# Optimization experiments

Hardware: AMD Instinct MI355X
Metric: run time of the kernel (lower is better)

Reference implementation:

```python
import jax, jax.numpy as jnp
import numpy as np

N = 262144   # nodes
E = 4194304  # edges (avg degree 16)
G = 1024     # graphs in batch
F_IN, F_GCN, F_DENSE = 3, 16, 16
NEG_SLOPE = 0.01  # nn.LeakyReLU default


def _leaky(x):
    return jax.nn.leaky_relu(x, NEG_SLOPE)


def _gcn_conv(x, W, b, src, dst, ew):
    """PyG GCNConv: h = x @ W; symmetric deg-norm with self-loops (weight 1);
    out[i] = sum_{(j->i)} norm_e * h[j] + (1/deg_i) * h[i] + b."""
    h = x @ W                                   # [N, out]
    deg = jax.ops.segment_sum(ew, dst, num_segments=N) + 1.0  # +1 from self-loop
    dinv = jnp.where(deg > 0, jax.lax.rsqrt(deg), 0.0)        # deg^{-1/2}
    norm = dinv[src] * ew * dinv[dst]           # [E]
    agg = jax.ops.segment_sum(h[src] * norm[:, None], dst, num_segments=N)
    agg = agg + h * (dinv * dinv)[:, None]      # self-loop message, norm = 1/deg
    return agg + b


def setup_inputs() -> dict:
    key = jax.random.key(0)
    ks = jax.random.split(key, 24)
    inp = {
        "X": jax.random.normal(ks[0], (N, F_IN), dtype=jnp.float32),
        "Edge_index": jax.random.randint(ks[1], (2, E), 0, N, dtype=jnp.int64) if jax.config.jax_enable_x64 else jax.random.randint(ks[1], (2, E), 0, N, dtype=jnp.int32),
        "Edge_weight": jax.random.uniform(ks[2], (E,), dtype=jnp.float32),
        "Batching": jnp.sort(jax.random.randint(ks[3], (N,), 0, G, dtype=jnp.int32)),
        "num_graphs": G,
    }
    def lin(k, fi, fo):
        kw, kb = jax.random.split(k)
        s = 1.0 / np.sqrt(fi)
        return (jax.random.uniform(kw, (fi, fo), minval=-s, maxval=s, dtype=jnp.float32),
                jax.random.uniform(kb, (fo,), minval=-s, maxval=s, dtype=jnp.float32))
    inp["W1"], inp["b1"] = lin(ks[4], F_IN, F_GCN)
    inp["W2"], inp["b2"] = lin(ks[5], F_GCN, F_GCN)
    inp["Wp1"], inp["bp1"] = lin(ks[6], F_GCN, F_DENSE)
    inp["Wp2"], inp["bp2"] = lin(ks[7], F_DENSE, F_DENSE)
    inp["Wp3"], inp["bp3"] = lin(ks[8], F_DENSE, 2)
    inp["Wt1"], inp["bt1"] = lin(ks[9], F_GCN, F_DENSE)
    inp["Wt2"], inp["bt2"] = lin(ks[10], F_DENSE, F_DENSE)
    inp["Wt3"], inp["bt3"] = lin(ks[11], F_DENSE, 2)
    return inp


def reference(X, Edge_index, Edge_weight, Batching, num_graphs,
              W1, b1, W2, b2,
              Wp1, bp1, Wp2, bp2, Wp3, bp3,
              Wt1, bt1, Wt2, bt2, Wt3, bt3):
    src, dst = Edge_index[0], Edge_index[1]
    out = _leaky(_gcn_conv(X, W1, b1, src, dst, Edge_weight))
    out = _leaky(_gcn_conv(out, W2, b2, src, dst, Edge_weight))
    # global mean pool over graphs
    sums = jax.ops.segment_sum(out, Batching, num_segments=num_graphs)
    cnt = jax.ops.segment_sum(jnp.ones((out.shape[0],), out.dtype), Batching,
                              num_segments=num_graphs)
    pooled = sums / jnp.maximum(cnt, 1.0)[:, None]   # [G, 16]
    Phi = _leaky(pooled @ Wp1 + bp1)
    Phi = _leaky(Phi @ Wp2 + bp2)
    Phi = Phi @ Wp3 + bp3
    Theta = _leaky(pooled @ Wt1 + bt1)
    Theta = _leaky(Theta @ Wt2 + bt2)
    Theta = Theta @ Wt3 + bt3
    return jnp.concatenate((Phi, Theta), axis=1)   # [G, 4]
```

## Files before the change

kernel.cpp:

```cpp
#include <hip/hip_runtime.h>


#define NBUCK 512
#define BCAP  10240
#define CHUNK 4096
#define NTILE 8
#define TSH   15
#define RCAP  20

__device__ __forceinline__ float leaky(float x) { return x > 0.f ? x : 0.01f * x; }

__global__ __launch_bounds__(256) void
binA_kernel(const int* __restrict__ src, const int* __restrict__ dst,
            const float* __restrict__ ew, int* __restrict__ bucketCursor,
            int2* __restrict__ coarse, int E) {
    __shared__ int lhist[NBUCK], lbase[NBUCK], lcur[NBUCK], gbase[NBUCK];
    __shared__ int tmp[256];
    __shared__ int2 stag[CHUNK];
    __shared__ unsigned short sbuck[CHUNK];
    int t = threadIdx.x;
    int base = blockIdx.x * CHUNK;
    for (int b = t; b < NBUCK; b += 256) { lhist[b] = 0; lcur[b] = 0; }
    __syncthreads();
    int n = min(CHUNK, E - base);
    int myDst[16], mySrc[16]; float myEw[16];
#pragma unroll
    for (int k = 0; k < 16; ++k) {
        int j = t + k * 256;
        if (j < n) {
            int d = dst[base + j];
            myDst[k] = d; mySrc[k] = src[base + j]; myEw[k] = ew[base + j];
            atomicAdd(&lhist[d >> 9], 1);
        } else myDst[k] = -1;
    }
    __syncthreads();
    tmp[t] = lhist[2 * t] + lhist[2 * t + 1];
    __syncthreads();
    for (int off = 1; off < 256; off <<= 1) {
        int v = (t >= off) ? tmp[t - off] : 0;
        __syncthreads();
        tmp[t] += v;
        __syncthreads();
    }
    int pb = (t == 0) ? 0 : tmp[t - 1];
    lbase[2 * t] = pb;
    lbase[2 * t + 1] = pb + lhist[2 * t];
    __syncthreads();
    for (int b = t; b < NBUCK; b += 256) {
        int c = lhist[b];
        gbase[b] = c ? atomicAdd(&bucketCursor[b], c) : 0;
    }
    for (int k = 0; k < 16; ++k) {
        int d = myDst[k];
        if (d >= 0) {
            int b = d >> 9;
            int p = lbase[b] + atomicAdd(&lcur[b], 1);
            stag[p] = make_int2(mySrc[k] | ((d & 511) << 18), __float_as_int(myEw[k]));
            sbuck[p] = (unsigned short)b;
        }
    }
    __syncthreads();
    for (int j = t; j < n; j += 256) {
        int b = sbuck[j];
        coarse[(size_t)b * BCAP + gbase[b] + (j - lbase[b])] = stag[j];
    }
}

__global__ void bscan_kernel(const int* __restrict__ bucketCursor,
                             int* __restrict__ bucketBase, int* __restrict__ row,
                             int N, int E) {
    __shared__ int s[NBUCK];
    int t = threadIdx.x;
    int v = bucketCursor[t];
    s[t] = v;
    __syncthreads();
    for (int off = 1; off < NBUCK; off <<= 1) {
        int x = (t >= off) ? s[t - off] : 0;
        __syncthreads();
        s[t] += x;
        __syncthreads();
    }
    bucketBase[t] = s[t] - v;
    if (t == 0) row[N] = E;
}

__global__ __launch_bounds__(512, 2) void
binB_kernel(const int* __restrict__ bucketCursor, const int* __restrict__ bucketBase,
            const int2* __restrict__ coarse, int2* __restrict__ edata,
            int* __restrict__ row, float* __restrict__ dinv,
            uint4* __restrict__ tcnt) {
    __shared__ int2 sedata[BCAP];
    __shared__ int loff[NBUCK * NTILE];
    __shared__ int tmp[512];
    int b = blockIdx.x, t = threadIdx.x;
    for (int i = t; i < NBUCK * NTILE; i += 512) loff[i] = 0;
    __syncthreads();
    int cnt = bucketCursor[b];
    int gb  = bucketBase[b];
    const int2* cb = coarse + (size_t)b * BCAP;
    int2 myE[RCAP]; int myKey[RCAP];
#pragma unroll
    for (int k = 0; k < RCAP; ++k) {
        int j = t + k * 512;
        if (j < cnt) {
            int2 e = cb[j];
            myE[k] = e;
            myKey[k] = (((e.x >> 18) & 511) << 3) | ((e.x & 0x3FFFF) >> TSH);
            atomicAdd(&loff[myKey[k]], 1);
        } else myKey[k] = -1;
    }
    __syncthreads();
    int base8 = t * 8, s = 0;
#pragma unroll
    for (int k = 0; k < 8; ++k) s += loff[base8 + k];
    tmp[t] = s;
    __syncthreads();
    for (int off = 1; off < 512; off <<= 1) {
        int v = (t >= off) ? tmp[t - off] : 0;
        __syncthreads();
        tmp[t] += v;
        __syncthreads();
    }
    int run = tmp[t] - s;
    int o[9];
#pragma unroll
    for (int k = 0; k < 8; ++k) { int v = loff[base8 + k]; o[k] = run; loff[base8 + k] = run; run += v; }
    o[8] = run;
    __syncthreads();
    int node = b * 512 + t;
    row[node] = gb + o[0];
    uint4 p;
    p.x = (unsigned)(o[1] - o[0]) | ((unsigned)(o[2] - o[1]) << 16);
    p.y = (unsigned)(o[3] - o[2]) | ((unsigned)(o[4] - o[3]) << 16);
    p.z = (unsigned)(o[5] - o[4]) | ((unsigned)(o[6] - o[5]) << 16);
    p.w = (unsigned)(o[7] - o[6]) | ((unsigned)(o[8] - o[7]) << 16);
    tcnt[node] = p;
#pragma unroll
    for (int k = 0; k < RCAP; ++k) {
        if (myKey[k] >= 0) {
            int pos = atomicAdd(&loff[myKey[k]], 1);
            sedata[pos] = make_int2(myE[k].x & 0x3FFFF, myE[k].y);
        }
    }
    __syncthreads();
    for (int j = t; j < cnt; j += 512) edata[gb + j] = sedata[j];
    float dsum = 0.f;
    for (int j = o[0]; j < o[8]; ++j) dsum += __int_as_float(sedata[j].y);
    dinv[node] = rsqrtf(1.0f + dsum);
}

__global__ void pack_kernel(const float* __restrict__ X, const float* __restrict__ dinv,
                            float4* __restrict__ Xp, int N) {
    int i = blockIdx.x * blockDim.x + threadIdx.x;
    if (i >= N) return;
    Xp[i] = make_float4(X[3 * i], X[3 * i + 1], X[3 * i + 2], dinv[i]);
}

__global__ __launch_bounds__(512) void
aggA_kernel(const int* __restrict__ row, const int2* __restrict__ edata,
            const float4* __restrict__ Xp, const float* __restrict__ W1,
            const float* __restrict__ b1, const float* __restrict__ W2,
            float* __restrict__ h2) {
    __shared__ float w1s[48];
    __shared__ float w[256];
    __shared__ float bb[16];
    __shared__ float sx[128][17];
    int t = threadIdx.x;
    if (t < 256) w[t] = W2[t];
    else if (t < 272) bb[t - 256] = b1[t - 256];
    else if (t >= 288 && t < 336) w1s[t - 288] = W1[t - 288];
    __syncthreads();
    int ln = t >> 2, l = t & 3;
    float w1r0[4], w1r1[4], w1r2[4];
#pragma unroll
    for (int c = 0; c < 4; ++c) {
        w1r0[c] = w1s[0 * 16 + 4 * l + c];
        w1r1[c] = w1s[1 * 16 + 4 * l + c];
        w1r2[c] = w1s[2 * 16 + 4 * l + c];
    }
    int iA = blockIdx.x * 256 + ln, iB = iA + 128;
    int eA = row[iA], eAend = row[iA + 1];
    int eB = row[iB], eBend = row[iB + 1];
    float4 xpA = Xp[iA], xpB = Xp[iB];
    float diA = xpA.w, diB = xpB.w;
    float accA[4], accB[4];
#pragma unroll
    for (int c = 0; c < 4; ++c) {
        accA[c] = (xpA.x * w1r0[c] + xpA.y * w1r1[c] + xpA.z * w1r2[c]) * diA;
        accB[c] = (xpB.x * w1r0[c] + xpB.y * w1r1[c] + xpB.z * w1r2[c]) * diB;
    }
    while (eA < eAend || eB < eBend) {
        if (eA < eAend) {
            int2 ed = edata[eA++];
            float4 xs = Xp[ed.x];
            float f = __int_as_float(ed.y) * xs.w;
            float f0 = xs.x * f, f1 = xs.y * f, f2 = xs.z * f;
#pragma unroll
            for (int c = 0; c < 4; ++c)
                accA[c] += f0 * w1r0[c] + f1 * w1r1[c] + f2 * w1r2[c];
        }
        if (eB < eBend) {
            int2 ed = edata[eB++];
            float4 xs = Xp[ed.x];
            float f = __int_as_float(ed.y) * xs.w;
            float f0 = xs.x * f, f1 = xs.y * f, f2 = xs.z * f;
#pragma unroll
            for (int c = 0; c < 4; ++c)
                accB[c] += f0 * w1r0[c] + f1 * w1r1[c] + f2 * w1r2[c];
        }
    }
    sx[ln][4 * l + 0] = leaky(diA * accA[0] + bb[4 * l + 0]);
    sx[ln][4 * l + 1] = leaky(diA * accA[1] + bb[4 * l + 1]);
    sx[ln][4 * l + 2] = leaky(diA * accA[2] + bb[4 * l + 2]);
    sx[ln][4 * l + 3] = leaky(diA * accA[3] + bb[4 * l + 3]);
    __syncthreads();
    {
        float a0 = 0.f, a1 = 0.f, a2 = 0.f, a3 = 0.f;
#pragma unroll
        for (int q = 0; q < 16; ++q) {
            float xv = sx[ln][q];
            a0 += xv * w[q * 16 + 4 * l + 0];
            a1 += xv * w[q * 16 + 4 * l + 1];
            a2 += xv * w[q * 16 + 4 * l + 2];
            a3 += xv * w[q * 16 + 4 * l + 3];
        }
        ((float4*)h2)[(size_t)iA * 4 + l] = make_float4(a0 * diA, a1 * diA, a2 * diA, a3 * diA);
    }
    __syncthreads();
    sx[ln][4 * l + 0] = leaky(diB * accB[0] + bb[4 * l + 0]);
    sx[ln][4 * l + 1] = leaky(diB * accB[1] + bb[4 * l + 1]);
    sx[ln][4 * l + 2] = leaky(diB * accB[2] + bb[4 * l + 2]);
    sx[ln][4 * l + 3] = leaky(diB * accB[3] + bb[4 * l + 3]);
    __syncthreads();
    {
        float a0 = 0.f, a1 = 0.f, a2 = 0.f, a3 = 0.f;
#pragma unroll
        for (int q = 0; q < 16; ++q) {
            float xv = sx[ln][q];
            a0 += xv * w[q * 16 + 4 * l + 0];
            a1 += xv * w[q * 16 + 4 * l + 1];
            a2 += xv * w[q * 16 + 4 * l + 2];
            a3 += xv * w[q * 16 + 4 * l + 3];
        }
        ((float4*)h2)[(size_t)iB * 4 + l] = make_float4(a0 * diB, a1 * diB, a2 * diB, a3 * diB);
    }
}

__global__ __launch_bounds__(512) void
aggB_kernel(const int* __restrict__ row, const uint4* __restrict__ tcnt,
            const int2* __restrict__ edata, const float* __restrict__ dinv,
            const float* __restrict__ h2prime, float* __restrict__ agg2) {
    int t = threadIdx.x;
    int ln = t >> 2, l = t & 3;
    int iA = blockIdx.x * 256 + ln, iB = iA + 128;
    const float4* hp = (const float4*)h2prime;
    int eA = row[iA], eB = row[iB];
    uint4 cAv = tcnt[iA], cBv = tcnt[iB];
    unsigned ca[4] = {cAv.x, cAv.y, cAv.z, cAv.w};
    unsigned cb[4] = {cBv.x, cBv.y, cBv.z, cBv.w};
    float diA = dinv[iA], diB = dinv[iB];
    float4 accA = hp[(size_t)iA * 4 + l];
    float4 accB = hp[(size_t)iB * 4 + l];
#pragma unroll
    for (int tt = 0; tt < NTILE; ++tt) {
        int nA = (ca[tt >> 1] >> ((tt & 1) * 16)) & 0xFFFF;
        int nB = (cb[tt >> 1] >> ((tt & 1) * 16)) & 0xFFFF;
        for (int e = eA + nA; eA < e; ++eA) {
            int2 ed = edata[eA];
            float ewv = __int_as_float(ed.y);
            float4 v = hp[(size_t)ed.x * 4 + l];
            accA.x += v.x * ewv; accA.y += v.y * ewv;
            accA.z += v.z * ewv; accA.w += v.w * ewv;
        }
        for (int e = eB + nB; eB < e; ++eB) {
            int2 ed = edata[eB];
            float ewv = __int_as_float(ed.y);
            float4 v = hp[(size_t)ed.x * 4 + l];
            accB.x += v.x * ewv; accB.y += v.y * ewv;
            accB.z += v.z * ewv; accB.w += v.w * ewv;
        }
        __syncthreads();
    }
    ((float4*)agg2)[(size_t)iA * 4 + l] =
        make_float4(accA.x * diA, accA.y * diA, accA.z * diA, accA.w * diA);
    ((float4*)agg2)[(size_t)iB * 4 + l] =
        make_float4(accB.x * diB, accB.y * diB, accB.z * diB, accB.w * diB);
}

__device__ void head_mlp(const float* pooled,
                         const float* __restrict__ Wa, const float* __restrict__ ba,
                         const float* __restrict__ Wb, const float* __restrict__ bb,
                         const float* __restrict__ Wc, const float* __restrict__ bc,
                         float* o) {
    float t[16], u[16];
#pragma unroll
    for (int f = 0; f < 16; ++f) {
        float a = ba[f];
        for (int k = 0; k < 16; ++k) a += pooled[k] * Wa[k * 16 + f];
        t[f] = leaky(a);
    }
#pragma unroll
    for (int f = 0; f < 16; ++f) {
        float a = bb[f];
        for (int k = 0; k < 16; ++k) a += t[k] * Wb[k * 16 + f];
        u[f] = leaky(a);
    }
    float o0 = bc[0], o1 = bc[1];
    for (int k = 0; k < 16; ++k) { o0 += u[k] * Wc[2 * k]; o1 += u[k] * Wc[2 * k + 1]; }
    o[0] = o0; o[1] = o1;
}

__global__ void pool_head_kernel(const float* __restrict__ agg2, const float* __restrict__ b2,
                                 const int* __restrict__ batching, int N,
                                 const float* __restrict__ Wp1, const float* __restrict__ bp1,
                                 const float* __restrict__ Wp2, const float* __restrict__ bp2,
                                 const float* __restrict__ Wp3, const float* __restrict__ bp3,
                                 const float* __restrict__ Wt1, const float* __restrict__ bt1,
                                 const float* __restrict__ Wt2, const float* __restrict__ bt2,
                                 const float* __restrict__ Wt3, const float* __restrict__ bt3,
                                 float* __restrict__ out) {
    int g = blockIdx.x;
    __shared__ int bounds[2];
    if (threadIdx.x < 2) {
        int v = g + (int)threadIdx.x;
        int lo = 0, hi = N;
        while (lo < hi) { int m = (lo + hi) >> 1; if (batching[m] < v) lo = m + 1; else hi = m; }
        bounds[threadIdx.x] = lo;
    }
    __syncthreads();
    int lo = bounds[0], hi = bounds[1];
    int f = threadIdx.x & 15, r = threadIdx.x >> 4;
    float bf = b2[f];
    float acc = 0.f;
    for (int i = lo + r; i < hi; i += 16) acc += leaky(agg2[(size_t)i * 16 + f] + bf);
    __shared__ float red[16][17];
    red[r][f] = acc;
    __syncthreads();
    __shared__ float pooled[16];
    if (r == 0) {
        float s = 0.f;
#pragma unroll
        for (int k = 0; k < 16; ++k) s += red[k][f];
        pooled[f] = s / fmaxf((float)(hi - lo), 1.0f);
    }
    __syncthreads();
    if (threadIdx.x == 0) {
        float o[2];
        head_mlp(pooled, Wp1, bp1, Wp2, bp2, Wp3, bp3, o);
        out[4 * g + 0] = o[0]; out[4 * g + 1] = o[1];
    } else if (threadIdx.x == 1) {
        float o[2];
        head_mlp(pooled, Wt1, bt1, Wt2, bt2, Wt3, bt3, o);
        out[4 * g + 2] = o[0]; out[4 * g + 3] = o[1];
    }
}

extern "C" void kernel_launch(void* const* d_in, const int* in_sizes, int n_in,
                              void* d_out, int out_size, void* d_ws, size_t ws_size,
                              hipStream_t stream) {
    const float* X        = (const float*)d_in[0];
    const int*   ei       = (const int*)d_in[1];
    const float* ew       = (const float*)d_in[2];
    const int*   batching = (const int*)d_in[3];
    const float* W1  = (const float*)d_in[5];  const float* b1  = (const float*)d_in[6];
    const float* W2  = (const float*)d_in[7];  const float* b2  = (const float*)d_in[8];
    const float* Wp1 = (const float*)d_in[9];  const float* bp1 = (const float*)d_in[10];
    const float* Wp2 = (const float*)d_in[11]; const float* bp2 = (const float*)d_in[12];
    const float* Wp3 = (const float*)d_in[13]; const float* bp3 = (const float*)d_in[14];
    const float* Wt1 = (const float*)d_in[15]; const float* bt1 = (const float*)d_in[16];
    const float* Wt2 = (const float*)d_in[17]; const float* bt2 = (const float*)d_in[18];
    const float* Wt3 = (const float*)d_in[19]; const float* bt3 = (const float*)d_in[20];

    const int N = in_sizes[3];
    const int E = in_sizes[2];
    const int G = out_size / 4;
    const int* src = ei;
    const int* dst = ei + E;

    char* ws = (char*)d_ws;
    size_t off = 0;
    int2*  edata = (int2*)(ws + off);  off += (size_t)E * 8;
    char*  regionA = ws + off;         off += (size_t)N * 64 * 3;
    int2*  coarse = (int2*)regionA;
    float* h2     = (float*)regionA;
    float* agg2   = (float*)(regionA + (size_t)N * 64);
    float4* Xp    = (float4*)(regionA + (size_t)N * 128);
    int*   bucketCursor = (int*)(ws + off); off += NBUCK * 4;
    int*   bucketBase   = (int*)(ws + off); off += NBUCK * 4;
    int*   row   = (int*)(ws + off);   off += (size_t)(N + 4) * 4;
    float* dinv  = (float*)(ws + off); off += (size_t)N * 4;
    uint4* tcnt  = (uint4*)(ws + off); off += (size_t)N * 16;
    float* out   = (float*)d_out;

    hipMemsetAsync(bucketCursor, 0, NBUCK * 4, stream);

    const int tb = 256;
    binA_kernel<<<(E + CHUNK - 1) / CHUNK, tb, 0, stream>>>(src, dst, ew, bucketCursor, coarse, E);
    bscan_kernel<<<1, NBUCK, 0, stream>>>(bucketCursor, bucketBase, row, N, E);
    binB_kernel<<<NBUCK, 512, 0, stream>>>(bucketCursor, bucketBase, coarse, edata, row, dinv, tcnt);
    pack_kernel<<<(N + tb - 1) / tb, tb, 0, stream>>>(X, dinv, Xp, N);
    aggA_kernel<<<N / 256, 512, 0, stream>>>(row, edata, Xp, W1, b1, W2, h2);
    aggB_kernel<<<N / 256, 512, 0, stream>>>(row, tcnt, edata, dinv, h2, agg2);
    pool_head_kernel<<<G, tb, 0, stream>>>(agg2, b2, batching, N,
                                           Wp1, bp1, Wp2, bp2, Wp3, bp3,
                                           Wt1, bt1, Wt2, bt2, Wt3, bt3, out);
}
```

Baseline: 382.4 us.

## Tile-synchronize first-layer gather and use nontemporal edge loads and output stores

The first GCN aggregation kernel now walks each node's edges in per-source-tile segments taken from the tcnt counts, with a block barrier after each tile. This mirrors the second aggregation kernel and keeps the block's gathers of Xp confined to one source range at a time, so they stay cache-resident. Both aggregation kernels also read edge records with nontemporal loads and write h2 and agg2 with nontemporal stores, to keep the streamed data from evicting the gathered feature rows. The extra barriers can stall warps whose nodes have uneven per-tile degrees.

```diff
diff --git a/kernel.cpp b/kernel.cpp
--- a/kernel.cpp
+++ b/kernel.cpp
@@ -9,6 +9,18 @@
 #define RCAP  20
 
 __device__ __forceinline__ float leaky(float x) { return x > 0.f ? x : 0.01f * x; }
+
+typedef float __attribute__((ext_vector_type(4))) f32x4;
+
+__device__ __forceinline__ void nt_store4(float a, float b, float c, float d, float* dst) {
+    f32x4 v = {a, b, c, d};
+    __builtin_nontemporal_store(v, (f32x4*)dst);
+}
+__device__ __forceinline__ void nt_edge(const int2* p, int& s, float& w) {
+    long long raw = __builtin_nontemporal_load((const long long*)p);
+    s = (int)(unsigned)(raw & 0xFFFFFFFFll);
+    w = __int_as_float((int)(raw >> 32));
+}
 
 __global__ __launch_bounds__(256) void
 binA_kernel(const int* __restrict__ src, const int* __restrict__ dst,
@@ -157,10 +169,10 @@
 }
 
 __global__ __launch_bounds__(512) void
-aggA_kernel(const int* __restrict__ row, const int2* __restrict__ edata,
-            const float4* __restrict__ Xp, const float* __restrict__ W1,
-            const float* __restrict__ b1, const float* __restrict__ W2,
-            float* __restrict__ h2) {
+aggA_kernel(const int* __restrict__ row, const uint4* __restrict__ tcnt,
+            const int2* __restrict__ edata, const float4* __restrict__ Xp,
+            const float* __restrict__ W1, const float* __restrict__ b1,
+            const float* __restrict__ W2, float* __restrict__ h2) {
     __shared__ float w1s[48];
     __shared__ float w[256];
     __shared__ float bb[16];
@@ -179,8 +191,10 @@
         w1r2[c] = w1s[2 * 16 + 4 * l + c];
     }
     int iA = blockIdx.x * 256 + ln, iB = iA + 128;
-    int eA = row[iA], eAend = row[iA + 1];
-    int eB = row[iB], eBend = row[iB + 1];
+    int eA = row[iA], eB = row[iB];
+    uint4 cAv = tcnt[iA], cBv = tcnt[iB];
+    unsigned ca[4] = {cAv.x, cAv.y, cAv.z, cAv.w};
+    unsigned cb[4] = {cBv.x, cBv.y, cBv.z, cBv.w};
     float4 xpA = Xp[iA], xpB = Xp[iB];
     float diA = xpA.w, diB = xpB.w;
     float accA[4], accB[4];
@@ -189,25 +203,29 @@
         accA[c] = (xpA.x * w1r0[c] + xpA.y * w1r1[c] + xpA.z * w1r2[c]) * diA;
         accB[c] = (xpB.x * w1r0[c] + xpB.y * w1r1[c] + xpB.z * w1r2[c]) * diB;
     }
-    while (eA < eAend || eB < eBend) {
-        if (eA < eAend) {
-            int2 ed = edata[eA++];
-            float4 xs = Xp[ed.x];
-            float f = __int_as_float(ed.y) * xs.w;
+#pragma unroll
+    for (int tt = 0; tt < NTILE; ++tt) {
+        int nA = (ca[tt >> 1] >> ((tt & 1) * 16)) & 0xFFFF;
+        int nB = (cb[tt >> 1] >> ((tt & 1) * 16)) & 0xFFFF;
+        for (int e = eA + nA; eA < e; ++eA) {
+            int s; float ewv; nt_edge(edata + eA, s, ewv);
+            float4 xs = Xp[s];
+            float f = ewv * xs.w;
             float f0 = xs.x * f, f1 = xs.y * f, f2 = xs.z * f;
 #pragma unroll
             for (int c = 0; c < 4; ++c)
                 accA[c] += f0 * w1r0[c] + f1 * w1r1[c] + f2 * w1r2[c];
         }
-        if (eB < eBend) {
-            int2 ed = edata[eB++];
-            float4 xs = Xp[ed.x];
-            float f = __int_as_float(ed.y) * xs.w;
+        for (int e = eB + nB; eB < e; ++eB) {
+            int s; float ewv; nt_edge(edata + eB, s, ewv);
+            float4 xs = Xp[s];
+            float f = ewv * xs.w;
             float f0 = xs.x * f, f1 = xs.y * f, f2 = xs.z * f;
 #pragma unroll
             for (int c = 0; c < 4; ++c)
                 accB[c] += f0 * w1r0[c] + f1 * w1r1[c] + f2 * w1r2[c];
         }
+        __syncthreads();
     }
     sx[ln][4 * l + 0] = leaky(diA * accA[0] + bb[4 * l + 0]);
     sx[ln][4 * l + 1] = leaky(diA * accA[1] + bb[4 * l + 1]);
@@ -224,7 +242,7 @@
             a2 += xv * w[q * 16 + 4 * l + 2];
             a3 += xv * w[q * 16 + 4 * l + 3];
         }
-        ((float4*)h2)[(size_t)iA * 4 + l] = make_float4(a0 * diA, a1 * diA, a2 * diA, a3 * diA);
+        nt_store4(a0 * diA, a1 * diA, a2 * diA, a3 * diA, h2 + (size_t)iA * 16 + l * 4);
     }
     __syncthreads();
     sx[ln][4 * l + 0] = leaky(diB * accB[0] + bb[4 * l + 0]);
@@ -242,7 +260,7 @@
             a2 += xv * w[q * 16 + 4 * l + 2];
             a3 += xv * w[q * 16 + 4 * l + 3];
         }
-        ((float4*)h2)[(size_t)iB * 4 + l] = make_float4(a0 * diB, a1 * diB, a2 * diB, a3 * diB);
+        nt_store4(a0 * diB, a1 * diB, a2 * diB, a3 * diB, h2 + (size_t)iB * 16 + l * 4);
     }
 }
 
@@ -266,25 +284,23 @@
         int nA = (ca[tt >> 1] >> ((tt & 1) * 16)) & 0xFFFF;
         int nB = (cb[tt >> 1] >> ((tt & 1) * 16)) & 0xFFFF;
         for (int e = eA + nA; eA < e; ++eA) {
-            int2 ed = edata[eA];
-            float ewv = __int_as_float(ed.y);
-            float4 v = hp[(size_t)ed.x * 4 + l];
+            int s; float ewv; nt_edge(edata + eA, s, ewv);
+            float4 v = hp[(size_t)s * 4 + l];
             accA.x += v.x * ewv; accA.y += v.y * ewv;
             accA.z += v.z * ewv; accA.w += v.w * ewv;
         }
         for (int e = eB + nB; eB < e; ++eB) {
-            int2 ed = edata[eB];
-            float ewv = __int_as_float(ed.y);
-            float4 v = hp[(size_t)ed.x * 4 + l];
+            int s; float ewv; nt_edge(edata + eB, s, ewv);
+            float4 v = hp[(size_t)s * 4 + l];
             accB.x += v.x * ewv; accB.y += v.y * ewv;
             accB.z += v.z * ewv; accB.w += v.w * ewv;
         }
         __syncthreads();
     }
-    ((float4*)agg2)[(size_t)iA * 4 + l] =
-        make_float4(accA.x * diA, accA.y * diA, accA.z * diA, accA.w * diA);
-    ((float4*)agg2)[(size_t)iB * 4 + l] =
-        make_float4(accB.x * diB, accB.y * diB, accB.z * diB, accB.w * diB);
+    nt_store4(accA.x * diA, accA.y * diA, accA.z * diA, accA.w * diA,
+              agg2 + (size_t)iA * 16 + l * 4);
+    nt_store4(accB.x * diB, accB.y * diB, accB.z * diB, accB.w * diB,
+              agg2 + (size_t)iB * 16 + l * 4);
 }
 
 __device__ void head_mlp(const float* pooled,
@@ -399,7 +415,7 @@
     bscan_kernel<<<1, NBUCK, 0, stream>>>(bucketCursor, bucketBase, row, N, E);
     binB_kernel<<<NBUCK, 512, 0, stream>>>(bucketCursor, bucketBase, coarse, edata, row, dinv, tcnt);
     pack_kernel<<<(N + tb - 1) / tb, tb, 0, stream>>>(X, dinv, Xp, N);
-    aggA_kernel<<<N / 256, 512, 0, stream>>>(row, edata, Xp, W1, b1, W2, h2);
+    aggA_kernel<<<N / 256, 512, 0, stream>>>(row, tcnt, edata, Xp, W1, b1, W2, h2);
     aggB_kernel<<<N / 256, 512, 0, stream>>>(row, tcnt, edata, dinv, h2, agg2);
     pool_head_kernel<<<G, tb, 0, stream>>>(agg2, b2, batching, N,
                                            Wp1, bp1, Wp2, bp2, Wp3, bp3,
```

Result: slower. 429.5 us (+12.3%).

## Enlarge binning blocks and tile aggA edge loop by source range with block sync

Applied to the files above, without the earlier changes.

The edge-binning kernel now runs 512 threads over 8192-edge chunks, so each bucket maps to one thread and the two-per-thread scan is dropped. The first aggregation kernel now walks each node's edges in eight source-range tiles, using per-tile counts already computed for aggB, with a block barrier after each tile. The barrier keeps the block's gathers of Xp within a narrow source window for better cache locality. In exchange it adds synchronization, and load imbalance inside a tile now stalls the whole block.

```diff
diff --git a/kernel.cpp b/kernel.cpp
--- a/kernel.cpp
+++ b/kernel.cpp
@@ -3,30 +3,31 @@
 
 #define NBUCK 512
 #define BCAP  10240
-#define CHUNK 4096
+#define CHUNK 8192
+#define APT   16
 #define NTILE 8
 #define TSH   15
 #define RCAP  20
 
 __device__ __forceinline__ float leaky(float x) { return x > 0.f ? x : 0.01f * x; }
 
-__global__ __launch_bounds__(256) void
+__global__ __launch_bounds__(512) void
 binA_kernel(const int* __restrict__ src, const int* __restrict__ dst,
             const float* __restrict__ ew, int* __restrict__ bucketCursor,
             int2* __restrict__ coarse, int E) {
     __shared__ int lhist[NBUCK], lbase[NBUCK], lcur[NBUCK], gbase[NBUCK];
-    __shared__ int tmp[256];
+    __shared__ int tmp[NBUCK];
     __shared__ int2 stag[CHUNK];
     __shared__ unsigned short sbuck[CHUNK];
     int t = threadIdx.x;
     int base = blockIdx.x * CHUNK;
-    for (int b = t; b < NBUCK; b += 256) { lhist[b] = 0; lcur[b] = 0; }
+    lhist[t] = 0; lcur[t] = 0;
     __syncthreads();
     int n = min(CHUNK, E - base);
-    int myDst[16], mySrc[16]; float myEw[16];
-#pragma unroll
-    for (int k = 0; k < 16; ++k) {
-        int j = t + k * 256;
+    int myDst[APT], mySrc[APT]; float myEw[APT];
+#pragma unroll
+    for (int k = 0; k < APT; ++k) {
+        int j = t + k * 512;
         if (j < n) {
             int d = dst[base + j];
             myDst[k] = d; mySrc[k] = src[base + j]; myEw[k] = ew[base + j];
@@ -34,23 +35,20 @@
         } else myDst[k] = -1;
     }
     __syncthreads();
-    tmp[t] = lhist[2 * t] + lhist[2 * t + 1];
-    __syncthreads();
-    for (int off = 1; off < 256; off <<= 1) {
+    int hv = lhist[t];
+    tmp[t] = hv;
+    __syncthreads();
+    for (int off = 1; off < NBUCK; off <<= 1) {
         int v = (t >= off) ? tmp[t - off] : 0;
         __syncthreads();
         tmp[t] += v;
         __syncthreads();
     }
-    int pb = (t == 0) ? 0 : tmp[t - 1];
-    lbase[2 * t] = pb;
-    lbase[2 * t + 1] = pb + lhist[2 * t];
-    __syncthreads();
-    for (int b = t; b < NBUCK; b += 256) {
-        int c = lhist[b];
-        gbase[b] = c ? atomicAdd(&bucketCursor[b], c) : 0;
-    }
-    for (int k = 0; k < 16; ++k) {
+    lbase[t] = tmp[t] - hv;
+    gbase[t] = hv ? atomicAdd(&bucketCursor[t], hv) : 0;
+    __syncthreads();
+#pragma unroll
+    for (int k = 0; k < APT; ++k) {
         int d = myDst[k];
         if (d >= 0) {
             int b = d >> 9;
@@ -60,7 +58,7 @@
         }
     }
     __syncthreads();
-    for (int j = t; j < n; j += 256) {
+    for (int j = t; j < n; j += 512) {
         int b = sbuck[j];
         coarse[(size_t)b * BCAP + gbase[b] + (j - lbase[b])] = stag[j];
     }
@@ -157,10 +155,10 @@
 }
 
 __global__ __launch_bounds__(512) void
-aggA_kernel(const int* __restrict__ row, const int2* __restrict__ edata,
-            const float4* __restrict__ Xp, const float* __restrict__ W1,
-            const float* __restrict__ b1, const float* __restrict__ W2,
-            float* __restrict__ h2) {
+aggA_kernel(const int* __restrict__ row, const uint4* __restrict__ tcnt,
+            const int2* __restrict__ edata, const float4* __restrict__ Xp,
+            const float* __restrict__ W1, const float* __restrict__ b1,
+            const float* __restrict__ W2, float* __restrict__ h2) {
     __shared__ float w1s[48];
     __shared__ float w[256];
     __shared__ float bb[16];
@@ -179,8 +177,10 @@
         w1r2[c] = w1s[2 * 16 + 4 * l + c];
     }
     int iA = blockIdx.x * 256 + ln, iB = iA + 128;
-    int eA = row[iA], eAend = row[iA + 1];
-    int eB = row[iB], eBend = row[iB + 1];
+    int eA = row[iA], eB = row[iB];
+    uint4 cAv = tcnt[iA], cBv = tcnt[iB];
+    unsigned ca[4] = {cAv.x, cAv.y, cAv.z, cAv.w};
+    unsigned cb[4] = {cBv.x, cBv.y, cBv.z, cBv.w};
     float4 xpA = Xp[iA], xpB = Xp[iB];
     float diA = xpA.w, diB = xpB.w;
     float accA[4], accB[4];
@@ -189,9 +189,12 @@
         accA[c] = (xpA.x * w1r0[c] + xpA.y * w1r1[c] + xpA.z * w1r2[c]) * diA;
         accB[c] = (xpB.x * w1r0[c] + xpB.y * w1r1[c] + xpB.z * w1r2[c]) * diB;
     }
-    while (eA < eAend || eB < eBend) {
-        if (eA < eAend) {
-            int2 ed = edata[eA++];
+#pragma unroll
+    for (int tt = 0; tt < NTILE; ++tt) {
+        int nA = (ca[tt >> 1] >> ((tt & 1) * 16)) & 0xFFFF;
+        int nB = (cb[tt >> 1] >> ((tt & 1) * 16)) & 0xFFFF;
+        for (int e = eA + nA; eA < e; ++eA) {
+            int2 ed = edata[eA];
             float4 xs = Xp[ed.x];
             float f = __int_as_float(ed.y) * xs.w;
             float f0 = xs.x * f, f1 = xs.y * f, f2 = xs.z * f;
@@ -199,8 +202,8 @@
             for (int c = 0; c < 4; ++c)
                 accA[c] += f0 * w1r0[c] + f1 * w1r1[c] + f2 * w1r2[c];
         }
-        if (eB < eBend) {
-            int2 ed = edata[eB++];
+        for (int e = eB + nB; eB < e; ++eB) {
+            int2 ed = edata[eB];
             float4 xs = Xp[ed.x];
             float f = __int_as_float(ed.y) * xs.w;
             float f0 = xs.x * f, f1 = xs.y * f, f2 = xs.z * f;
@@ -208,6 +211,7 @@
             for (int c = 0; c < 4; ++c)
                 accB[c] += f0 * w1r0[c] + f1 * w1r1[c] + f2 * w1r2[c];
         }
+        __syncthreads();
     }
     sx[ln][4 * l + 0] = leaky(diA * accA[0] + bb[4 * l + 0]);
     sx[ln][4 * l + 1] = leaky(diA * accA[1] + bb[4 * l + 1]);
@@ -395,11 +399,11 @@
     hipMemsetAsync(bucketCursor, 0, NBUCK * 4, stream);
 
     const int tb = 256;
-    binA_kernel<<<(E + CHUNK - 1) / CHUNK, tb, 0, stream>>>(src, dst, ew, bucketCursor, coarse, E);
+    binA_kernel<<<(E + CHUNK - 1) / CHUNK, 512, 0, stream>>>(src, dst, ew, bucketCursor, coarse, E);
     bscan_kernel<<<1, NBUCK, 0, stream>>>(bucketCursor, bucketBase, row, N, E);
     binB_kernel<<<NBUCK, 512, 0, stream>>>(bucketCursor, bucketBase, coarse, edata, row, dinv, tcnt);
     pack_kernel<<<(N + tb - 1) / tb, tb, 0, stream>>>(X, dinv, Xp, N);
-    aggA_kernel<<<N / 256, 512, 0, stream>>>(row, edata, Xp, W1, b1, W2, h2);
+    aggA_kernel<<<N / 256, 512, 0, stream>>>(row, tcnt, edata, Xp, W1, b1, W2, h2);
     aggB_kernel<<<N / 256, 512, 0, stream>>>(row, tcnt, edata, dinv, h2, agg2);
     pool_head_kernel<<<G, tb, 0, stream>>>(agg2, b2, batching, N,
                                            Wp1, bp1, Wp2, bp2, Wp3, bp3,
```

After: 348.4 us. 8.9% less time.
